# Performance work log

Measured on AMD Instinct MI355X. Metric: run time of the kernel, lower is better.

## Reference

```python
import jax, jax.numpy as jnp
import numpy as np

B, S, E, WIN = 8, 2048, 512, 11  # batch, seq_len, emb_dim, window_size (odd)
PAD_VAL = 0.0  # padding_idx used as constant pad value in F.pad


def setup_inputs() -> dict:
    key = jax.random.key(0)
    k1, k2, k3 = jax.random.split(key, 3)
    x = jax.random.normal(k1, (B, S, E), dtype=jnp.float32)
    lim = 1.0 / np.sqrt(E * WIN)  # torch Linear default init bound
    # One independent Linear per timestep (deepcopy clones): stacked weights/bias
    W = jax.random.uniform(k2, (S, WIN, WIN * E), minval=-lim, maxval=lim, dtype=jnp.float32)
    b = jax.random.uniform(k3, (S, WIN), minval=-lim, maxval=lim, dtype=jnp.float32)
    return {"x": x, "W": W, "b": b}


def reference(x, W, b):
    ww = WIN // 2
    # pad sequence dim on both sides with padding_idx
    padded = jnp.pad(x, ((0, 0), (ww, ww), (0, 0)), constant_values=PAD_VAL)  # [B, S+2ww, E]
    # gather all sliding windows at once: windows[b,t,j,:] = padded[b, t+j, :]
    idx = jnp.arange(S)[:, None] + jnp.arange(WIN)[None, :]
    windows = padded[:, idx, :]
    flat = windows.reshape(B, S, WIN * E)                     # flattened window per position
    gates = jax.nn.sigmoid(jnp.einsum('bsf,swf->bsw', flat, W) + b)
    # gate * embeddings, sum over window, tanh
    score = jnp.einsum('bsw,bswe->bse', gates, windows)       # [B, S, E]
    return jnp.tanh(score)
```

## Files before the change

### kernel.cpp

```cpp
#include <hip/hip_runtime.h>
#include <math.h>

#define B_    8
#define S_    2048
#define E_    512
#define WIN_  11
#define WW    5
#define F4C   1408
#define E4C   128
#define PSTR  (B_ * WIN_)

template <int CTRL, int RMASK>
__device__ __forceinline__ float dpp_add(float v) {
    int sh = __builtin_amdgcn_update_dpp(0, __float_as_int(v),
                                         CTRL, RMASK, 0xF, true);
    return v + __int_as_float(sh);
}
__device__ __forceinline__ float wave_sum63(float v) {
    v = dpp_add<0x111, 0xF>(v);
    v = dpp_add<0x112, 0xF>(v);
    v = dpp_add<0x114, 0xF>(v);
    v = dpp_add<0x118, 0xF>(v);
    v = dpp_add<0x142, 0xA>(v);
    v = dpp_add<0x143, 0xC>(v);
    return v;
}

__device__ __forceinline__ float tanh_fast(float v) {
    const float e = __expf(v + v);
    return 1.f - 2.f / (e + 1.f);
}

__global__ __launch_bounds__(256)
void win_attn_fused(const float* __restrict__ x,
                    const float* __restrict__ W,
                    const float* __restrict__ bias,
                    float* __restrict__ out)
{
    const int bid  = blockIdx.x;
    const int s    = (bid & 7) * (S_ / 8) + (bid >> 3);
    const int tid  = threadIdx.x;
    const int wid  = tid >> 6;
    const int lane = tid & 63;

    const float4* __restrict__ X4 = reinterpret_cast<const float4*>(x);
    const float4* __restrict__ Ws = reinterpret_cast<const float4*>(W)
                                    + (size_t)s * (WIN_ * F4C);

    __shared__ float4 Wbuf[WIN_ * E4C];
    __shared__ float4 xbuf[B_ * E4C];
    __shared__ float gates[PSTR];

    const int w0   = wid * 3;
    const int wcnt = (wid == 3) ? 2 : 3;

    float acc[B_][3];
    #pragma unroll
    for (int b = 0; b < B_; ++b)
        #pragma unroll
        for (int j = 0; j < 3; ++j) acc[b][j] = 0.f;

    const int wpLo = (s >= WW) ? 0 : (WW - s);
    const int wpHi = (WIN_ < S_ + WW - s) ? WIN_ : (S_ + WW - s);

    #pragma unroll 1
    for (int wp = wpLo; wp < wpHi; ++wp) {
        const int row = s - WW + wp;

        #pragma unroll
        for (int j = 0; j < 6; ++j) {
            const int m = j * 256 + tid;
            if (j < 5 || wid < 2) {
                const int w  = m >> 7;
                const int e4 = m & 127;
                const float4* src = Ws + (size_t)w * F4C + wp * E4C + e4;
                __builtin_amdgcn_global_load_lds(
                    (const __attribute__((address_space(1))) void*)src,
                    (__attribute__((address_space(3))) void*)&Wbuf[m],
                    16, 0, 0);
            }
        }
        #pragma unroll
        for (int j = 0; j < 4; ++j) {
            const int m = j * 256 + tid;
            const int b  = m >> 7;
            const int e4 = m & 127;
            const float4* src = X4 + ((size_t)b * S_ + row) * E4C + e4;
            __builtin_amdgcn_global_load_lds(
                (const __attribute__((address_space(1))) void*)src,
                (__attribute__((address_space(3))) void*)&xbuf[m],
                16, 0, 0);
        }
        __syncthreads();

        float4 wv[3][2];
        #pragma unroll
        for (int j = 0; j < 3; ++j)
            if (j < wcnt) {
                wv[j][0] = Wbuf[(w0 + j) * E4C + lane];
                wv[j][1] = Wbuf[(w0 + j) * E4C + lane + 64];
            }

        #pragma unroll
        for (int half = 0; half < 2; ++half) {
            float4 xv[4][2];
            #pragma unroll
            for (int bb = 0; bb < 4; ++bb) {
                const int b = half * 4 + bb;
                xv[bb][0] = xbuf[b * E4C + lane];
                xv[bb][1] = xbuf[b * E4C + lane + 64];
            }
            #pragma unroll
            for (int bb = 0; bb < 4; ++bb) {
                const int b = half * 4 + bb;
                #pragma unroll
                for (int j = 0; j < 3; ++j)
                    if (j < wcnt) {
                        float a = acc[b][j];
                        a = fmaf(xv[bb][0].x, wv[j][0].x, a);
                        a = fmaf(xv[bb][0].y, wv[j][0].y, a);
                        a = fmaf(xv[bb][0].z, wv[j][0].z, a);
                        a = fmaf(xv[bb][0].w, wv[j][0].w, a);
                        a = fmaf(xv[bb][1].x, wv[j][1].x, a);
                        a = fmaf(xv[bb][1].y, wv[j][1].y, a);
                        a = fmaf(xv[bb][1].z, wv[j][1].z, a);
                        a = fmaf(xv[bb][1].w, wv[j][1].w, a);
                        acc[b][j] = a;
                    }
            }
        }
        __syncthreads();
    }

    #pragma unroll
    for (int b = 0; b < B_; ++b)
        #pragma unroll
        for (int j = 0; j < 3; ++j)
            if (j < wcnt) acc[b][j] = wave_sum63(acc[b][j]);

    if (lane == 63) {
        #pragma unroll
        for (int b = 0; b < B_; ++b)
            #pragma unroll
            for (int j = 0; j < 3; ++j)
                if (j < wcnt) gates[b * WIN_ + w0 + j] = acc[b][j];
    }
    __syncthreads();

    if (tid < PSTR) {
        const int w = tid % WIN_;
        const float v = gates[tid] + bias[s * WIN_ + w];
        gates[tid] = 1.f / (1.f + __expf(-v));
    }
    __syncthreads();

    float4* __restrict__ OUT4 = reinterpret_cast<float4*>(out);
    #pragma unroll
    for (int it = 0; it < 4; ++it) {
        const int i  = tid + (it << 8);
        const int b  = i >> 7;
        const int e4 = i & 127;
        float4 sc = make_float4(0.f, 0.f, 0.f, 0.f);
        #pragma unroll
        for (int w = 0; w < WIN_; ++w) {
            const int r = s - WW + w;
            if (r >= 0 && r < S_) {
                const float g   = gates[b * WIN_ + w];
                const float4 xv = X4[((size_t)b * S_ + r) * E4C + e4];
                sc.x = fmaf(g, xv.x, sc.x);
                sc.y = fmaf(g, xv.y, sc.y);
                sc.z = fmaf(g, xv.z, sc.z);
                sc.w = fmaf(g, xv.w, sc.w);
            }
        }
        float4 o;
        o.x = tanh_fast(sc.x);
        o.y = tanh_fast(sc.y);
        o.z = tanh_fast(sc.z);
        o.w = tanh_fast(sc.w);
        OUT4[((size_t)b * S_ + s) * E4C + e4] = o;
    }
}

extern "C" void kernel_launch(void* const* d_in, const int* in_sizes, int n_in,
                              void* d_out, int out_size, void* d_ws, size_t ws_size,
                              hipStream_t stream)
{
    const float* x    = (const float*)d_in[0];
    const float* W    = (const float*)d_in[1];
    const float* bias = (const float*)d_in[2];
    float* out        = (float*)d_out;

    win_attn_fused<<<dim3(S_), dim3(256), 0, stream>>>(x, W, bias, out);
}
```

Baseline: 143.0 us.

## Double-buffer LDS staging of W and x rows to overlap loads with compute

Adds a second LDS buffer for the weight and x tiles and prefetches the next window position while the current one is computed. Waits use explicit vmcnt counts and raw s_barrier in place of __syncthreads. This aims to hide global-to-LDS load latency behind the FMA work. In exchange it doubles LDS use, which may reduce occupancy, and it depends on hand-counted vmcnt values being correct.

```diff
diff --git a/kernel.cpp b/kernel.cpp
--- a/kernel.cpp
+++ b/kernel.cpp
@@ -47,12 +47,40 @@
     const float4* __restrict__ Ws = reinterpret_cast<const float4*>(W)
                                     + (size_t)s * (WIN_ * F4C);
 
-    __shared__ float4 Wbuf[WIN_ * E4C];
-    __shared__ float4 xbuf[B_ * E4C];
+    __shared__ float4 Wbuf[2][WIN_ * E4C];
+    __shared__ float4 xbuf[2][B_ * E4C];
     __shared__ float gates[PSTR];
 
     const int w0   = wid * 3;
     const int wcnt = (wid == 3) ? 2 : 3;
+
+    auto STAGE = [&](int buf, int wp) {
+        const int row = s - WW + wp;
+        #pragma unroll
+        for (int j = 0; j < 10; ++j) {
+            const int m = j * 256 + tid;
+            if (j < 9 || tid < 128) {
+                if (m < 1408) {
+                    const int w  = m >> 7;
+                    const int e4 = m & 127;
+                    const float4* src = Ws + (size_t)w * F4C + wp * E4C + e4;
+                    __builtin_amdgcn_global_load_lds(
+                        (const __attribute__((address_space(1))) void*)src,
+                        (__attribute__((address_space(3))) void*)&Wbuf[buf][m],
+                        16, 0, 0);
+                } else {
+                    const int n  = m - 1408;
+                    const int b  = n >> 7;
+                    const int e4 = n & 127;
+                    const float4* src = X4 + ((size_t)b * S_ + row) * E4C + e4;
+                    __builtin_amdgcn_global_load_lds(
+                        (const __attribute__((address_space(1))) void*)src,
+                        (__attribute__((address_space(3))) void*)&xbuf[buf][n],
+                        16, 0, 0);
+                }
+            }
+        }
+    };
 
     float acc[B_][3];
     #pragma unroll
@@ -63,42 +91,29 @@
     const int wpLo = (s >= WW) ? 0 : (WW - s);
     const int wpHi = (WIN_ < S_ + WW - s) ? WIN_ : (S_ + WW - s);
 
+    STAGE(0, wpLo);
+    int cur = 0;
+
     #pragma unroll 1
     for (int wp = wpLo; wp < wpHi; ++wp) {
-        const int row = s - WW + wp;
-
-        #pragma unroll
-        for (int j = 0; j < 6; ++j) {
-            const int m = j * 256 + tid;
-            if (j < 5 || wid < 2) {
-                const int w  = m >> 7;
-                const int e4 = m & 127;
-                const float4* src = Ws + (size_t)w * F4C + wp * E4C + e4;
-                __builtin_amdgcn_global_load_lds(
-                    (const __attribute__((address_space(1))) void*)src,
-                    (__attribute__((address_space(3))) void*)&Wbuf[m],
-                    16, 0, 0);
-            }
-        }
-        #pragma unroll
-        for (int j = 0; j < 4; ++j) {
-            const int m = j * 256 + tid;
-            const int b  = m >> 7;
-            const int e4 = m & 127;
-            const float4* src = X4 + ((size_t)b * S_ + row) * E4C + e4;
-            __builtin_amdgcn_global_load_lds(
-                (const __attribute__((address_space(1))) void*)src,
-                (__attribute__((address_space(3))) void*)&xbuf[m],
-                16, 0, 0);
-        }
-        __syncthreads();
+        const bool more = (wp + 1 < wpHi);
+        if (more) STAGE(cur ^ 1, wp + 1);
+
+        if (more) {
+            if (wid < 2) asm volatile("s_waitcnt vmcnt(10)" ::: "memory");
+            else         asm volatile("s_waitcnt vmcnt(9)"  ::: "memory");
+        } else {
+            asm volatile("s_waitcnt vmcnt(0)" ::: "memory");
+        }
+        __builtin_amdgcn_s_barrier();
+        __builtin_amdgcn_sched_barrier(0);
 
         float4 wv[3][2];
         #pragma unroll
         for (int j = 0; j < 3; ++j)
             if (j < wcnt) {
-                wv[j][0] = Wbuf[(w0 + j) * E4C + lane];
-                wv[j][1] = Wbuf[(w0 + j) * E4C + lane + 64];
+                wv[j][0] = Wbuf[cur][(w0 + j) * E4C + lane];
+                wv[j][1] = Wbuf[cur][(w0 + j) * E4C + lane + 64];
             }
 
         #pragma unroll
@@ -107,8 +122,8 @@
             #pragma unroll
             for (int bb = 0; bb < 4; ++bb) {
                 const int b = half * 4 + bb;
-                xv[bb][0] = xbuf[b * E4C + lane];
-                xv[bb][1] = xbuf[b * E4C + lane + 64];
+                xv[bb][0] = xbuf[cur][b * E4C + lane];
+                xv[bb][1] = xbuf[cur][b * E4C + lane + 64];
             }
             #pragma unroll
             for (int bb = 0; bb < 4; ++bb) {
@@ -129,7 +144,9 @@
                     }
             }
         }
-        __syncthreads();
+        __builtin_amdgcn_sched_barrier(0);
+        __builtin_amdgcn_s_barrier();
+        cur ^= 1;
     }
 
     #pragma unroll
```

Result: slower. 157.1 us (+9.9%).
